# Optimization experiments

Hardware: AMD Instinct MI355X
Metric: run time of the kernel (lower is better)

The kernel has to match this reference:

```python
import jax, jax.numpy as jnp
import numpy as np

NUM_HEADS = 24
HEAD_DIM = 128
DIM = NUM_HEADS * HEAD_DIM  # 3072
EPS = 1e-6


def rms_norm(x, g):
    # x: [b, h, s, d], g: [d]
    var = jnp.mean(jnp.square(x.astype(jnp.float32)), axis=-1, keepdims=True)
    return (x.astype(jnp.float32) * jax.lax.rsqrt(var + EPS)).astype(x.dtype) * g


def apply_rope(x, cos, sin):
    # x: [b, h, s, d]; cos/sin: [s, d//2]; complex multiply on interleaved pairs
    b, h, s, d = x.shape
    xr = x.reshape(b, h, s, d // 2, 2)
    x0, x1 = xr[..., 0], xr[..., 1]
    c = cos[None, None, :, :]
    sn = sin[None, None, :, :]
    o0 = x0 * c - x1 * sn
    o1 = x0 * sn + x1 * c
    return jnp.stack([o0, o1], axis=-1).reshape(b, h, s, d)


def split_heads(x):
    # [b, s, h*d] -> [b, h, s, d]
    b, s, _ = x.shape
    return x.reshape(b, s, NUM_HEADS, HEAD_DIM).transpose(0, 2, 1, 3)


def setup_inputs() -> dict:
    key = jax.random.key(0)
    ks = jax.random.split(key, 16)
    b, s_img, s_txt = 1, 2048, 256
    image = jax.random.normal(ks[0], (b, s_img, DIM), jnp.float32)
    text = jax.random.normal(ks[1], (b, s_txt, DIM), jnp.float32)
    # rotary freqs: angles = pos * inv_freq
    half = HEAD_DIM // 2
    inv_freq = 1.0 / (10000.0 ** (np.arange(half, dtype=np.float32) / half))
    ang_i = np.arange(s_img, dtype=np.float32)[:, None] * inv_freq[None, :]
    ang_t = np.arange(s_txt, dtype=np.float32)[:, None] * inv_freq[None, :]
    img_cos, img_sin = jnp.cos(jnp.asarray(ang_i)), jnp.sin(jnp.asarray(ang_i))
    txt_cos, txt_sin = jnp.cos(jnp.asarray(ang_t)), jnp.sin(jnp.asarray(ang_t))
    sc = 1.0 / np.sqrt(DIM)
    Wqkv = jax.random.normal(ks[2], (DIM, 3 * DIM), jnp.float32) * sc
    bqkv = jnp.zeros((3 * DIM,), jnp.float32)
    Wadd = jax.random.normal(ks[3], (DIM, 3 * DIM), jnp.float32) * sc
    badd = jnp.zeros((3 * DIM,), jnp.float32)
    gq = jnp.ones((HEAD_DIM,), jnp.float32)
    gk = jnp.ones((HEAD_DIM,), jnp.float32)
    gaq = jnp.ones((HEAD_DIM,), jnp.float32)
    gak = jnp.ones((HEAD_DIM,), jnp.float32)
    Wout = jax.random.normal(ks[4], (DIM, DIM), jnp.float32) * sc
    bout = jnp.zeros((DIM,), jnp.float32)
    Waddout = jax.random.normal(ks[5], (DIM, DIM), jnp.float32) * sc
    baddout = jnp.zeros((DIM,), jnp.float32)
    return dict(image=image, text=text, img_cos=img_cos, img_sin=img_sin,
                txt_cos=txt_cos, txt_sin=txt_sin, Wqkv=Wqkv, bqkv=bqkv,
                Wadd=Wadd, badd=badd, gq=gq, gk=gk, gaq=gaq, gak=gak,
                Wout=Wout, bout=bout, Waddout=Waddout, baddout=baddout)


def reference(image, text, img_cos, img_sin, txt_cos, txt_sin,
              Wqkv, bqkv, Wadd, badd, gq, gk, gaq, gak,
              Wout, bout, Waddout, baddout):
    seq_txt = text.shape[1]
    img_qkv = image @ Wqkv + bqkv
    img_q, img_k, img_v = jnp.split(img_qkv, 3, axis=-1)
    txt_qkv = text @ Wadd + badd
    txt_q, txt_k, txt_v = jnp.split(txt_qkv, 3, axis=-1)

    img_q, img_k, img_v = split_heads(img_q), split_heads(img_k), split_heads(img_v)
    txt_q, txt_k, txt_v = split_heads(txt_q), split_heads(txt_k), split_heads(txt_v)

    img_q, img_k = rms_norm(img_q, gq), rms_norm(img_k, gk)
    txt_q, txt_k = rms_norm(txt_q, gaq), rms_norm(txt_k, gak)

    img_q = apply_rope(img_q, img_cos, img_sin)
    img_k = apply_rope(img_k, img_cos, img_sin)
    txt_q = apply_rope(txt_q, txt_cos, txt_sin)
    txt_k = apply_rope(txt_k, txt_cos, txt_sin)

    # joint attention: text tokens first, then image tokens
    q = jnp.concatenate([txt_q, img_q], axis=2)  # [b, h, S, d]
    k = jnp.concatenate([txt_k, img_k], axis=2)
    v = jnp.concatenate([txt_v, img_v], axis=2)

    scale = 1.0 / np.sqrt(HEAD_DIM)
    scores = jnp.einsum('bhqd,bhkd->bhqk', q, k) * scale
    probs = jax.nn.softmax(scores, axis=-1)
    attn = jnp.einsum('bhqk,bhkd->bhqd', probs, v)
    b, h, S, d = attn.shape
    attn = attn.transpose(0, 2, 1, 3).reshape(b, S, h * d)  # [b, S, dim]

    txt_out = attn[:, :seq_txt, :]
    img_out = attn[:, seq_txt:, :]
    img_out = img_out @ Wout + bout
    txt_out = txt_out @ Waddout + baddout
    return img_out, txt_out
```

## Files before the change

### kernel.cpp

```cpp
#include <hip/hip_runtime.h>

#define NH 24
#define HD 128
#define DM 3072
#define DM3 9216
#define STXT 256
#define SIMG 2048
#define SALL 2304

typedef __attribute__((ext_vector_type(8))) short bfrag;
typedef __attribute__((ext_vector_type(4))) float ffrag;

__device__ __forceinline__ unsigned short f2bf(float f) {
  unsigned int x = __builtin_bit_cast(unsigned int, f);
  x += 0x7fffu + ((x >> 16) & 1u);
  return (unsigned short)(x >> 16);
}

__device__ __forceinline__ void gload16(void* lds, const void* g) {
  __builtin_amdgcn_global_load_lds((const __attribute__((address_space(1))) unsigned int*)g,
                                   (__attribute__((address_space(3))) unsigned int*)lds, 16, 0, 0);
}

__global__ __launch_bounds__(256) void cast_kernel(const float* __restrict__ in,
                                                   unsigned short* __restrict__ out) {
  int i = blockIdx.x * 256 + threadIdx.x;
  float4 a = ((const float4*)in)[2 * i];
  float4 b = ((const float4*)in)[2 * i + 1];
  uint4 o;
  o.x = (unsigned)f2bf(a.x) | ((unsigned)f2bf(a.y) << 16);
  o.y = (unsigned)f2bf(a.z) | ((unsigned)f2bf(a.w) << 16);
  o.z = (unsigned)f2bf(b.x) | ((unsigned)f2bf(b.y) << 16);
  o.w = (unsigned)f2bf(b.z) | ((unsigned)f2bf(b.w) << 16);
  ((uint4*)out)[i] = o;
}

__global__ __launch_bounds__(256) void transpose_cast_kernel(const float* __restrict__ W,
                                                             unsigned short* __restrict__ Wt,
                                                             int K, int N) {
  __shared__ __align__(16) unsigned short tile[64 * 72];
  int k0 = blockIdx.y * 64, n0 = blockIdx.x * 64;
  int t = threadIdx.x;
  int rr = t >> 4, cc = (t & 15) * 4;
#pragma unroll
  for (int p = 0; p < 4; ++p) {
    int k = rr + p * 16;
    float4 v = *(const float4*)&W[(size_t)(k0 + k) * N + n0 + cc];
    tile[(cc + 0) * 72 + k] = f2bf(v.x);
    tile[(cc + 1) * 72 + k] = f2bf(v.y);
    tile[(cc + 2) * 72 + k] = f2bf(v.z);
    tile[(cc + 3) * 72 + k] = f2bf(v.w);
  }
  __syncthreads();
  int n = t >> 2, c = (t & 3) * 16;
  float4* dst = (float4*)&Wt[(size_t)(n0 + n) * K + k0 + c];
  dst[0] = *(float4*)&tile[n * 72 + c];
  dst[1] = *(float4*)&tile[n * 72 + c + 8];
}

#define STAGE256(tt, c)                                                                          \
  {                                                                                              \
    const size_t kof = (size_t)(tt)*64;                                                          \
    _Pragma("unroll") for (int hf = 0; hf < 2; ++hf) {                                           \
      _Pragma("unroll") for (int i = 0; i < 2; ++i) {                                            \
        gload16(&SA[c][hf][i * 4096 + sdst], Asrc + (size_t)(hf * 128 + i * 64) * K + kof);      \
        gload16(&SB[c][hf][i * 4096 + sdst], Bsrc + (size_t)(hf * 128 + i * 64) * K + kof);      \
      }                                                                                          \
    }                                                                                            \
  }

#define RDA(QM)                                                                       \
  _Pragma("unroll") for (int mi = 0; mi < 4; ++mi) {                                  \
    a_[mi * 2 + 0] = *(const bfrag*)&Ab[((QM)*64 + mi * 16 + l16) * 64 + ck0];        \
    a_[mi * 2 + 1] = *(const bfrag*)&Ab[((QM)*64 + mi * 16 + l16) * 64 + ck1];        \
  }

#define RDB(QN, DST)                                                                  \
  _Pragma("unroll") for (int ni = 0; ni < 2; ++ni) {                                  \
    DST[ni * 2 + 0] = *(const bfrag*)&Bb[((QN)*32 + ni * 16 + l16) * 64 + ck0];       \
    DST[ni * 2 + 1] = *(const bfrag*)&Bb[((QN)*32 + ni * 16 + l16) * 64 + ck1];       \
  }

#define MQUAD(QM, QN, BOP)                                                            \
  _Pragma("unroll") for (int mi = 0; mi < 4; ++mi) {                                  \
    _Pragma("unroll") for (int ni = 0; ni < 2; ++ni) {                                \
      _Pragma("unroll") for (int kk = 0; kk < 2; ++kk) {                              \
        acc[(QM)*4 + mi][(QN)*2 + ni] = __builtin_amdgcn_mfma_f32_16x16x32_bf16(      \
            a_[mi * 2 + kk], BOP[ni * 2 + kk], acc[(QM)*4 + mi][(QN)*2 + ni], 0, 0, 0); \
      }                                                                               \
    }                                                                                 \
  }

__global__ __launch_bounds__(512, 2) void gemm256(const unsigned short* __restrict__ A,
                                                  const unsigned short* __restrict__ Bt_txt,
                                                  const unsigned short* __restrict__ Bt_img,
                                                  const float* __restrict__ bias_txt,
                                                  const float* __restrict__ bias_img,
                                                  int N, int K, int ncols, int mode,
                                                  float* __restrict__ qkvf,
                                                  unsigned short* __restrict__ vtb,
                                                  float* __restrict__ out_txt,
                                                  float* __restrict__ out_img) {
  __shared__ __align__(16) unsigned short SA[2][2][8192];
  __shared__ __align__(16) unsigned short SB[2][2][8192];
  const int tid = threadIdx.x;
  const int wave = tid >> 6, lane = tid & 63, quad = lane >> 4, l16 = lane & 15;
  const int wr = wave >> 2, wc = wave & 3;
  const int nwg = gridDim.x;
  const int q8 = nwg >> 3, r8 = nwg & 7;
  const int xcd = blockIdx.x & 7, idx = blockIdx.x >> 3;
  const int wg = (xcd < r8 ? xcd * (q8 + 1) : r8 * (q8 + 1) + (xcd - r8) * q8) + idx;
  const int m0 = (wg / ncols) * 256, n0 = (wg % ncols) * 256;
  const unsigned short* Bt = (m0 == 0) ? Bt_txt : Bt_img;
  const float* bias = (m0 == 0) ? bias_txt : bias_img;

  const int srow = wave * 8 + (lane >> 3);
  const int scs = ((lane & 7) ^ (srow & 7)) * 8;
  const int sdst = wave * 512 + lane * 8;
  const unsigned short* Asrc = A + (size_t)(m0 + srow) * K + scs;
  const unsigned short* Bsrc = Bt + (size_t)(n0 + srow) * K + scs;

  const int rsw = l16 & 7;
  const int ck0 = (quad ^ rsw) * 8;
  const int ck1 = ((quad + 4) ^ rsw) * 8;

  ffrag zf = {0.f, 0.f, 0.f, 0.f};
  ffrag acc[8][4];
#pragma unroll
  for (int i = 0; i < 8; ++i)
#pragma unroll
    for (int j = 0; j < 4; ++j) acc[i][j] = zf;

  const int NT = K >> 6;
  STAGE256(0, 0);
  STAGE256(1, 1);

  for (int t = 0; t < NT; ++t) {
    const int cur = t & 1;
    if (t + 1 < NT) {
      asm volatile("s_waitcnt vmcnt(8)" ::: "memory");
    } else {
      asm volatile("s_waitcnt vmcnt(0)" ::: "memory");
    }
    __builtin_amdgcn_sched_barrier(0);
    __builtin_amdgcn_s_barrier();
    __builtin_amdgcn_sched_barrier(0);

    const unsigned short* Ab = &SA[cur][wr][0];
    const unsigned short* Bb = &SB[cur][wc >> 1][(wc & 1) * 4096];
    bfrag a_[8], b0_[4], b1_[4];

    RDA(0);
    RDB(0, b0_);
    __builtin_amdgcn_s_barrier();
    asm volatile("s_waitcnt lgkmcnt(0)" ::: "memory");
    __builtin_amdgcn_sched_barrier(0);
    __builtin_amdgcn_s_setprio(1);
    MQUAD(0, 0, b0_);
    __builtin_amdgcn_s_setprio(0);
    __builtin_amdgcn_s_barrier();

    RDB(1, b1_);
    __builtin_amdgcn_s_barrier();
    asm volatile("s_waitcnt lgkmcnt(0)" ::: "memory");
    __builtin_amdgcn_sched_barrier(0);
    __builtin_amdgcn_s_setprio(1);
    MQUAD(0, 1, b1_);
    __builtin_amdgcn_s_setprio(0);
    __builtin_amdgcn_s_barrier();

    RDA(1);
    __builtin_amdgcn_s_barrier();
    asm volatile("s_waitcnt lgkmcnt(0)" ::: "memory");
    __builtin_amdgcn_sched_barrier(0);
    __builtin_amdgcn_s_setprio(1);
    MQUAD(1, 0, b0_);
    __builtin_amdgcn_s_setprio(0);
    __builtin_amdgcn_s_barrier();
    __builtin_amdgcn_sched_barrier(0);

    if (t + 2 < NT) STAGE256(t + 2, cur);
    __builtin_amdgcn_sched_barrier(0);
    __builtin_amdgcn_s_setprio(1);
    MQUAD(1, 1, b1_);
    __builtin_amdgcn_s_setprio(0);
  }

#pragma unroll
  for (int a = 0; a < 8; ++a) {
    const int rowb = m0 + wr * 128 + (a >> 2) * 64 + (a & 3) * 16 + quad * 4;
#pragma unroll
    for (int b = 0; b < 4; ++b) {
      const int gn = n0 + wc * 64 + (b >> 1) * 32 + (b & 1) * 16 + l16;
      const float bv = bias[gn];
#pragma unroll
      for (int r = 0; r < 4; ++r) {
        float v = acc[a][b][r] + bv;
        int gm = rowb + r;
        if (mode == 2) {
          if (gm < STXT)
            out_txt[(size_t)gm * N + gn] = v;
          else
            out_img[(size_t)(gm - STXT) * N + gn] = v;
        } else {
          int which = gn / DM;
          int rr2 = gn - which * DM;
          int head = rr2 >> 7, d = rr2 & 127;
          if (which < 2)
            qkvf[(((size_t)which * NH + head) * SALL + gm) * HD + d] = v;
          else
            vtb[((size_t)head * HD + d) * SALL + gm] = f2bf(v);
        }
      }
    }
  }
}

__global__ __launch_bounds__(256) void norm_rope_kernel(
    const float* __restrict__ qkvf, const float* __restrict__ gq, const float* __restrict__ gk,
    const float* __restrict__ gaq, const float* __restrict__ gak,
    const float* __restrict__ img_cos, const float* __restrict__ img_sin,
    const float* __restrict__ txt_cos, const float* __restrict__ txt_sin,
    unsigned short* __restrict__ Qb, unsigned short* __restrict__ Kb) {
  int wave = threadIdx.x >> 6, lane = threadIdx.x & 63;
  int row = blockIdx.x * 4 + wave;
  int which = row / (NH * SALL);
  int rem = row - which * (NH * SALL);
  int s = rem % SALL;
  float2 v = *(const float2*)&qkvf[(size_t)row * HD + lane * 2];
  float ss = v.x * v.x + v.y * v.y;
#pragma unroll
  for (int m = 1; m < 64; m <<= 1) ss += __shfl_xor(ss, m);
  float rinv = rsqrtf(ss * (1.0f / 128.0f) + 1e-6f);
  bool is_txt = s < STXT;
  int pos = is_txt ? s : s - STXT;
  const float* g = (which == 0) ? (is_txt ? gaq : gq) : (is_txt ? gak : gk);
  const float* ct = is_txt ? txt_cos : img_cos;
  const float* st = is_txt ? txt_sin : img_sin;
  float c = ct[pos * 64 + lane], sn = st[pos * 64 + lane];
  float x0 = v.x * rinv * g[lane * 2];
  float x1 = v.y * rinv * g[lane * 2 + 1];
  float o0 = x0 * c - x1 * sn;
  float o1 = x0 * sn + x1 * c;
  unsigned short* out = (which == 0 ? Qb : Kb) + (size_t)rem * HD + lane * 2;
  *(unsigned int*)out = (unsigned)f2bf(o0) | ((unsigned)f2bf(o1) << 16);
}

__global__ __launch_bounds__(256) void flash_kernel(const unsigned short* __restrict__ Q,
                                                    const unsigned short* __restrict__ Kg,
                                                    const unsigned short* __restrict__ Vt,
                                                    unsigned short* __restrict__ attn) {
  __shared__ __align__(16) unsigned short Kl[64 * 128];
  __shared__ __align__(16) unsigned short Vl[128 * 64];
  __shared__ __align__(16) unsigned short Pl[4 * 16 * 64];
  int bid = blockIdx.x;
  int g = (bid & 7) * 108 + (bid >> 3);
  const int h = g / 36;
  const int qb = (g - h * 36) * 64;
  const int tid = threadIdx.x;
  const int wave = tid >> 6, lane = tid & 63, quad = lane >> 4, l16 = lane & 15;
  const int l7 = l16 & 7;

  const unsigned short* qrow = Q + ((size_t)h * SALL + qb + wave * 16 + l16) * HD;
  bfrag aq[4];
#pragma unroll
  for (int kk = 0; kk < 4; ++kk) aq[kk] = *(const bfrag*)&qrow[kk * 32 + quad * 8];

  const unsigned short* Kh = Kg + (size_t)h * SALL * HD;
  const unsigned short* Vh = Vt + (size_t)h * HD * SALL;

  const int kr = tid >> 4, kc = tid & 15;
  const int vr = tid >> 3, vc = tid & 7;
  const int kswz = kc ^ (kr & 7);
  const int vswz = vc ^ (vr & 7);

  ffrag zf = {0.f, 0.f, 0.f, 0.f};
  ffrag o[8];
#pragma unroll
  for (int i = 0; i < 8; ++i) o[i] = zf;
  float m_r[4] = {-__builtin_inff(), -__builtin_inff(), -__builtin_inff(), -__builtin_inff()};
  float l_r[4] = {0.f, 0.f, 0.f, 0.f};
  const float sc = 0.08838834764831845f * 1.4426950408889634f;

  bfrag kreg[4], vreg[4];
#pragma unroll
  for (int p = 0; p < 4; ++p) {
    kreg[p] = *(const bfrag*)&Kh[(size_t)(kr + p * 16) * HD + kc * 8];
    vreg[p] = *(const bfrag*)&Vh[(size_t)(vr + p * 32) * SALL + vc * 8];
  }

  for (int t = 0; t < SALL / 64; ++t) {
    __syncthreads();
#pragma unroll
    for (int p = 0; p < 4; ++p) {
      *(bfrag*)&Kl[(kr + p * 16) * 128 + kswz * 8] = kreg[p];
      *(bfrag*)&Vl[(vr + p * 32) * 64 + vswz * 8] = vreg[p];
    }
    __syncthreads();

    if (t + 1 < SALL / 64) {
      int kn = (t + 1) * 64;
#pragma unroll
      for (int p = 0; p < 4; ++p) {
        kreg[p] = *(const bfrag*)&Kh[(size_t)(kn + kr + p * 16) * HD + kc * 8];
        vreg[p] = *(const bfrag*)&Vh[(size_t)(vr + p * 32) * SALL + kn + vc * 8];
      }
    }

    ffrag s_[4];
#pragma unroll
    for (int nt = 0; nt < 4; ++nt) s_[nt] = zf;
#pragma unroll
    for (int kk = 0; kk < 4; ++kk) {
#pragma unroll
      for (int nt = 0; nt < 4; ++nt) {
        bfrag kf = *(const bfrag*)&Kl[(nt * 16 + l16) * 128 + ((kk * 4 + quad) ^ l7) * 8];
        s_[nt] = __builtin_amdgcn_mfma_f32_16x16x32_bf16(aq[kk], kf, s_[nt], 0, 0, 0);
      }
    }
#pragma unroll
    for (int nt = 0; nt < 4; ++nt)
#pragma unroll
      for (int r = 0; r < 4; ++r) s_[nt][r] *= sc;

    float alpha[4];
#pragma unroll
    for (int r = 0; r < 4; ++r) {
      float mx = fmaxf(fmaxf(s_[0][r], s_[1][r]), fmaxf(s_[2][r], s_[3][r]));
#pragma unroll
      for (int msk = 1; msk < 16; msk <<= 1) mx = fmaxf(mx, __shfl_xor(mx, msk));
      float mnew = fmaxf(m_r[r], mx);
      alpha[r] = exp2f(m_r[r] - mnew);
      m_r[r] = mnew;
      float rs = 0.f;
#pragma unroll
      for (int nt = 0; nt < 4; ++nt) {
        float p = exp2f(s_[nt][r] - mnew);
        s_[nt][r] = p;
        rs += p;
      }
#pragma unroll
      for (int msk = 1; msk < 16; msk <<= 1) rs += __shfl_xor(rs, msk);
      l_r[r] = l_r[r] * alpha[r] + rs;
    }
#pragma unroll
    for (int dt = 0; dt < 8; ++dt)
#pragma unroll
      for (int r = 0; r < 4; ++r) o[dt][r] *= alpha[r];
#pragma unroll
    for (int r = 0; r < 4; ++r) {
      int prow = quad * 4 + r;
#pragma unroll
      for (int nt = 0; nt < 4; ++nt)
        Pl[wave * 1024 + prow * 64 + ((nt * 16 + l16) ^ ((prow & 7) << 3))] = f2bf(s_[nt][r]);
    }

    bfrag pf0 = *(const bfrag*)&Pl[wave * 1024 + l16 * 64 + ((quad)     ^ l7) * 8];
    bfrag pf1 = *(const bfrag*)&Pl[wave * 1024 + l16 * 64 + ((quad + 4) ^ l7) * 8];
#pragma unroll
    for (int dt = 0; dt < 8; ++dt) {
      bfrag vf0 = *(const bfrag*)&Vl[(dt * 16 + l16) * 64 + ((quad)     ^ l7) * 8];
      bfrag vf1 = *(const bfrag*)&Vl[(dt * 16 + l16) * 64 + ((quad + 4) ^ l7) * 8];
      o[dt] = __builtin_amdgcn_mfma_f32_16x16x32_bf16(pf0, vf0, o[dt], 0, 0, 0);
      o[dt] = __builtin_amdgcn_mfma_f32_16x16x32_bf16(pf1, vf1, o[dt], 0, 0, 0);
    }
  }

  float linv[4];
#pragma unroll
  for (int r = 0; r < 4; ++r) linv[r] = 1.0f / l_r[r];
#pragma unroll
  for (int dt = 0; dt < 8; ++dt) {
#pragma unroll
    for (int r = 0; r < 4; ++r) {
      int s = qb + wave * 16 + quad * 4 + r;
      attn[(size_t)s * DM + h * HD + dt * 16 + l16] = f2bf(o[dt][r] * linv[r]);
    }
  }
}

extern "C" void kernel_launch(void* const* d_in, const int* in_sizes, int n_in,
                              void* d_out, int out_size, void* d_ws, size_t ws_size,
                              hipStream_t stream) {
  const float* image = (const float*)d_in[0];
  const float* text = (const float*)d_in[1];
  const float* img_cos = (const float*)d_in[2];
  const float* img_sin = (const float*)d_in[3];
  const float* txt_cos = (const float*)d_in[4];
  const float* txt_sin = (const float*)d_in[5];
  const float* Wqkv = (const float*)d_in[6];
  const float* bqkv = (const float*)d_in[7];
  const float* Wadd = (const float*)d_in[8];
  const float* badd = (const float*)d_in[9];
  const float* gq = (const float*)d_in[10];
  const float* gk = (const float*)d_in[11];
  const float* gaq = (const float*)d_in[12];
  const float* gak = (const float*)d_in[13];
  const float* Wout = (const float*)d_in[14];
  const float* bout = (const float*)d_in[15];
  const float* Waddout = (const float*)d_in[16];
  const float* baddout = (const float*)d_in[17];

  char* ws = (char*)d_ws;
  size_t off = 0;
  unsigned short* x_bf = (unsigned short*)(ws + off); off += (size_t)SALL * DM * 2;
  unsigned short* attn = x_bf;
  unsigned short* Wqkv_t = (unsigned short*)(ws + off); off += (size_t)DM3 * DM * 2;
  unsigned short* Wadd_t = (unsigned short*)(ws + off); off += (size_t)DM3 * DM * 2;
  unsigned short* Wout_t = (unsigned short*)(ws + off); off += (size_t)DM * DM * 2;
  unsigned short* Waddout_t = (unsigned short*)(ws + off); off += (size_t)DM * DM * 2;
  float* qkvf = (float*)(ws + off); off += (size_t)2 * NH * SALL * HD * 4;
  unsigned short* Qb = (unsigned short*)(ws + off); off += (size_t)NH * SALL * HD * 2;
  unsigned short* Kb = (unsigned short*)(ws + off); off += (size_t)NH * SALL * HD * 2;
  unsigned short* Vtb = (unsigned short*)(ws + off); off += (size_t)NH * HD * SALL * 2;
  if (off > ws_size) return;

  cast_kernel<<<STXT * DM / 2048, 256, 0, stream>>>(text, x_bf);
  cast_kernel<<<SIMG * DM / 2048, 256, 0, stream>>>(image, x_bf + (size_t)STXT * DM);
  transpose_cast_kernel<<<dim3(DM3 / 64, DM / 64), 256, 0, stream>>>(Wqkv, Wqkv_t, DM, DM3);
  transpose_cast_kernel<<<dim3(DM3 / 64, DM / 64), 256, 0, stream>>>(Wadd, Wadd_t, DM, DM3);
  transpose_cast_kernel<<<dim3(DM / 64, DM / 64), 256, 0, stream>>>(Wout, Wout_t, DM, DM);
  transpose_cast_kernel<<<dim3(DM / 64, DM / 64), 256, 0, stream>>>(Waddout, Waddout_t, DM, DM);

  gemm256<<<dim3((DM3 / 256) * (SALL / 256)), 512, 0, stream>>>(
      x_bf, Wadd_t, Wqkv_t, badd, bqkv, DM3, DM, DM3 / 256, 0, qkvf, Vtb, nullptr, nullptr);

  norm_rope_kernel<<<2 * NH * SALL / 4, 256, 0, stream>>>(qkvf, gq, gk, gaq, gak, img_cos,
                                                          img_sin, txt_cos, txt_sin, Qb, Kb);

  flash_kernel<<<dim3(SALL / 64 * NH), 256, 0, stream>>>(Qb, Kb, Vtb, attn);

  gemm256<<<dim3((DM / 256) * (SALL / 256)), 512, 0, stream>>>(
      attn, Waddout_t, Wout_t, baddout, bout, DM, DM, DM / 256, 2, nullptr, nullptr,
      (float*)d_out + (size_t)SIMG * DM, (float*)d_out);
}
```

Before: 991.6 us.

## Software-pipeline LDS fragment reads across K tiles and cut GEMM barriers

Rewrites the gemm256 main loop so each tile prefetches the next tile's A/B LDS fragments while the last MFMA quadrants of the current tile run. A and B fragments rotate through double register sets (a0_/a1_, bX/bY), and the loop is unrolled by two. Per-tile barriers drop from several to one, placed after a full vmcnt(0) wait, and staging of tile t+2 is issued at the end of the tile. This aims to hide LDS read latency behind MFMA work and cut synchronisation stalls, at the cost of more fragment registers, the loss of the partial vmcnt(8) overlap, and an assumption that the tile count is even.

```diff
diff --git a/kernel.cpp b/kernel.cpp
--- a/kernel.cpp
+++ b/kernel.cpp
@@ -69,26 +69,65 @@
     }                                                                                            \
   }
 
-#define RDA(QM)                                                                       \
-  _Pragma("unroll") for (int mi = 0; mi < 4; ++mi) {                                  \
-    a_[mi * 2 + 0] = *(const bfrag*)&Ab[((QM)*64 + mi * 16 + l16) * 64 + ck0];        \
-    a_[mi * 2 + 1] = *(const bfrag*)&Ab[((QM)*64 + mi * 16 + l16) * 64 + ck1];        \
-  }
-
-#define RDB(QN, DST)                                                                  \
-  _Pragma("unroll") for (int ni = 0; ni < 2; ++ni) {                                  \
-    DST[ni * 2 + 0] = *(const bfrag*)&Bb[((QN)*32 + ni * 16 + l16) * 64 + ck0];       \
-    DST[ni * 2 + 1] = *(const bfrag*)&Bb[((QN)*32 + ni * 16 + l16) * 64 + ck1];       \
-  }
-
-#define MQUAD(QM, QN, BOP)                                                            \
-  _Pragma("unroll") for (int mi = 0; mi < 4; ++mi) {                                  \
-    _Pragma("unroll") for (int ni = 0; ni < 2; ++ni) {                                \
-      _Pragma("unroll") for (int kk = 0; kk < 2; ++kk) {                              \
-        acc[(QM)*4 + mi][(QN)*2 + ni] = __builtin_amdgcn_mfma_f32_16x16x32_bf16(      \
-            a_[mi * 2 + kk], BOP[ni * 2 + kk], acc[(QM)*4 + mi][(QN)*2 + ni], 0, 0, 0); \
-      }                                                                               \
-    }                                                                                 \
+#define RD_A(DST, AB, QM)                                                                 \
+  _Pragma("unroll") for (int mi = 0; mi < 4; ++mi) {                                      \
+    DST[mi * 2 + 0] = *(const bfrag*)&(AB)[((QM)*64 + mi * 16 + l16) * 64 + ck0];         \
+    DST[mi * 2 + 1] = *(const bfrag*)&(AB)[((QM)*64 + mi * 16 + l16) * 64 + ck1];         \
+  }
+
+#define RD_B(DST, BB_, QN)                                                                \
+  _Pragma("unroll") for (int ni = 0; ni < 2; ++ni) {                                      \
+    DST[ni * 2 + 0] = *(const bfrag*)&(BB_)[((QN)*32 + ni * 16 + l16) * 64 + ck0];        \
+    DST[ni * 2 + 1] = *(const bfrag*)&(BB_)[((QN)*32 + ni * 16 + l16) * 64 + ck1];        \
+  }
+
+#define MQUAD(QM, QN, AV, BV)                                                             \
+  _Pragma("unroll") for (int mi = 0; mi < 4; ++mi) {                                      \
+    _Pragma("unroll") for (int ni = 0; ni < 2; ++ni) {                                    \
+      _Pragma("unroll") for (int kk = 0; kk < 2; ++kk) {                                  \
+        acc[(QM)*4 + mi][(QN)*2 + ni] = __builtin_amdgcn_mfma_f32_16x16x32_bf16(          \
+            AV[mi * 2 + kk], BV[ni * 2 + kk], acc[(QM)*4 + mi][(QN)*2 + ni], 0, 0, 0);    \
+      }                                                                                   \
+    }                                                                                     \
+  }
+
+#define TILE256(TT, CUR, BAv, BBv)                                                        \
+  {                                                                                       \
+    const unsigned short* Ab = &SA[CUR][wr][0];                                           \
+    const unsigned short* Bb = &SB[CUR][wc >> 1][(wc & 1) * 4096];                        \
+    const unsigned short* Abn = &SA[(CUR) ^ 1][wr][0];                                    \
+    const unsigned short* Bbn = &SB[(CUR) ^ 1][wc >> 1][(wc & 1) * 4096];                 \
+                                       \
+    asm volatile("s_waitcnt lgkmcnt(0)" ::: "memory");                      \
+    __builtin_amdgcn_sched_barrier(0);                                                    \
+    RD_B(BBv, Bb, 1);                                                                     \
+    __builtin_amdgcn_s_setprio(1);                                                        \
+    MQUAD(0, 0, a0_, BAv);                                                                \
+    __builtin_amdgcn_s_setprio(0);                                                        \
+                                                           \
+    asm volatile("s_waitcnt lgkmcnt(0)" ::: "memory");                         \
+    __builtin_amdgcn_sched_barrier(0);                                                    \
+    RD_A(a1_, Ab, 1);                                                                     \
+    __builtin_amdgcn_s_setprio(1);                                                        \
+    MQUAD(0, 1, a0_, BBv);                                                                \
+    __builtin_amdgcn_s_setprio(0);                                                        \
+                              \
+    asm volatile("s_waitcnt lgkmcnt(0)" ::: "memory");                         \
+    __builtin_amdgcn_sched_barrier(0);                                                    \
+    if ((TT) + 1 < NT) {                                                                  \
+      asm volatile("s_waitcnt vmcnt(0)" ::: "memory");          \
+      __builtin_amdgcn_s_barrier();                    \
+      RD_A(a0_, Abn, 0);                                                                  \
+    }                                                                                     \
+    __builtin_amdgcn_s_setprio(1);                                                        \
+    MQUAD(1, 1, a1_, BBv);                                                                \
+    __builtin_amdgcn_s_setprio(0);                                                        \
+                             \
+    if ((TT) + 1 < NT) RD_B(BBv, Bbn, 0);                                                 \
+    __builtin_amdgcn_s_setprio(1);                                                        \
+    MQUAD(1, 0, a1_, BAv);                                                                \
+    __builtin_amdgcn_s_setprio(0);                                                        \
+    if ((TT) + 2 < NT) STAGE256((TT) + 2, CUR);                                           \
   }
 
 __global__ __launch_bounds__(512, 2) void gemm256(const unsigned short* __restrict__ A,
@@ -132,58 +171,22 @@
     for (int j = 0; j < 4; ++j) acc[i][j] = zf;
 
   const int NT = K >> 6;
+  bfrag a0_[8], a1_[8], bX[4], bY[4];
+
   STAGE256(0, 0);
   STAGE256(1, 1);
-
-  for (int t = 0; t < NT; ++t) {
-    const int cur = t & 1;
-    if (t + 1 < NT) {
-      asm volatile("s_waitcnt vmcnt(8)" ::: "memory");
-    } else {
-      asm volatile("s_waitcnt vmcnt(0)" ::: "memory");
-    }
-    __builtin_amdgcn_sched_barrier(0);
-    __builtin_amdgcn_s_barrier();
-    __builtin_amdgcn_sched_barrier(0);
-
-    const unsigned short* Ab = &SA[cur][wr][0];
-    const unsigned short* Bb = &SB[cur][wc >> 1][(wc & 1) * 4096];
-    bfrag a_[8], b0_[4], b1_[4];
-
-    RDA(0);
-    RDB(0, b0_);
-    __builtin_amdgcn_s_barrier();
-    asm volatile("s_waitcnt lgkmcnt(0)" ::: "memory");
-    __builtin_amdgcn_sched_barrier(0);
-    __builtin_amdgcn_s_setprio(1);
-    MQUAD(0, 0, b0_);
-    __builtin_amdgcn_s_setprio(0);
-    __builtin_amdgcn_s_barrier();
-
-    RDB(1, b1_);
-    __builtin_amdgcn_s_barrier();
-    asm volatile("s_waitcnt lgkmcnt(0)" ::: "memory");
-    __builtin_amdgcn_sched_barrier(0);
-    __builtin_amdgcn_s_setprio(1);
-    MQUAD(0, 1, b1_);
-    __builtin_amdgcn_s_setprio(0);
-    __builtin_amdgcn_s_barrier();
-
-    RDA(1);
-    __builtin_amdgcn_s_barrier();
-    asm volatile("s_waitcnt lgkmcnt(0)" ::: "memory");
-    __builtin_amdgcn_sched_barrier(0);
-    __builtin_amdgcn_s_setprio(1);
-    MQUAD(1, 0, b0_);
-    __builtin_amdgcn_s_setprio(0);
-    __builtin_amdgcn_s_barrier();
-    __builtin_amdgcn_sched_barrier(0);
-
-    if (t + 2 < NT) STAGE256(t + 2, cur);
-    __builtin_amdgcn_sched_barrier(0);
-    __builtin_amdgcn_s_setprio(1);
-    MQUAD(1, 1, b1_);
-    __builtin_amdgcn_s_setprio(0);
+  asm volatile("s_waitcnt vmcnt(8)" ::: "memory");
+  __builtin_amdgcn_s_barrier();
+  {
+    const unsigned short* Ab0 = &SA[0][wr][0];
+    const unsigned short* Bb0 = &SB[0][wc >> 1][(wc & 1) * 4096];
+    RD_A(a0_, Ab0, 0);
+    RD_B(bX, Bb0, 0);
+  }
+
+  for (int t = 0; t < NT; t += 2) {
+    TILE256(t, 0, bX, bY);
+    TILE256(t + 1, 1, bY, bX);
   }
 
 #pragma unroll
```

Result: faster. 939.6 us (-5.2%).
